# Optimization experiments

Hardware: AMD Instinct MI355X
Metric: run time of the kernel (lower is better)

Reference implementation:

```python
import jax, jax.numpy as jnp
import numpy as np


def _pair_indices(n_beads):
    # Replicates the torch loop ordering: all pairs at offset 1, then offset 2, ...
    i_list, j_list = [], []
    for off in range(1, n_beads):
        i = np.arange(n_beads - off)
        i_list.append(i)
        j_list.append(i + off)
    return np.concatenate(i_list), np.concatenate(j_list)


def setup_inputs() -> dict:
    key = jax.random.key(0)
    data = jax.random.normal(key, (4096, 128, 3), dtype=jnp.float32)
    return {"data": data}


def _features(data):
    n = data.shape[1]
    i_idx, j_idx = _pair_indices(n)  # static numpy index arrays

    # All pairwise distances, ordered by bead offset (matches torch loop order)
    dvec = data[:, j_idx, :] - data[:, i_idx, :]          # [B, P, 3]
    distances = jnp.linalg.norm(dvec, axis=2)             # [B, P]

    # Adjacent bond vectors: x[j+1] - x[j]
    adj = data[:, 1:, :] - data[:, :-1, :]                # [B, n-1, 3]

    # Planar angles over consecutive bond-vector pairs
    a0, a1 = adj[:, : n - 2, :], adj[:, 1 : n - 1, :]
    angles = jnp.arccos(
        jnp.sum(a0 * a1, axis=2)
        / jnp.linalg.norm(a0, axis=2)
        / jnp.linalg.norm(a1, axis=2)
    )                                                     # [B, n-2]

    # Dihedrals
    cpa = jnp.cross(a0, a1, axis=2)                       # [B, n-2, 3]
    plane = jnp.cross(cpa[:, 1 : n - 2, :], adj[:, 1 : n - 2, :], axis=2)  # [B, n-3, 3]
    c0, c1 = cpa[:, : n - 3, :], cpa[:, 1 : n - 2, :]
    nc0 = jnp.linalg.norm(c0, axis=2)
    dihedral_cos = jnp.sum(c0 * c1, axis=2) / nc0 / jnp.linalg.norm(c1, axis=2)
    p0 = plane[:, : n - 3, :]
    dihedral_sin = jnp.sum(c0 * p0, axis=2) / nc0 / jnp.linalg.norm(p0, axis=2)

    return jnp.concatenate([distances, angles, dihedral_cos, dihedral_sin], axis=1)


def reference(data):
    return _features(data)
```

## Files before the change

### kernel.cpp

```cpp
#include <hip/hip_runtime.h>
#include <math.h>

constexpr int NB    = 128;
constexpr int NPAIR = NB * (NB - 1) / 2;
constexpr int NANG  = NB - 2;
constexpr int NDIH  = NB - 3;
constexpr int ROW   = NPAIR + NANG + 2 * NDIH;

__global__ __launch_bounds__(128) void protein_feat_kernel(
        const float* __restrict__ data, float* __restrict__ out) {
    __shared__ float4 s4[NB];
    const int b = blockIdx.x;
    const int t = threadIdx.x;
    const float* src = data + (size_t)b * (NB * 3);

    s4[t] = make_float4(src[3 * t], src[3 * t + 1], src[3 * t + 2], 0.0f);
    __syncthreads();

    float* orow = out + (size_t)b * ROW;

    float px[4], py[4], pz[4];
    #pragma unroll
    for (int k = 0; k < 4; ++k) {
        int idx = t - k; if (idx < 0) idx = 0;
        float4 v = s4[idx];
        px[k] = v.x; py[k] = v.y; pz[k] = v.z;
    }

    int base = 0;
    for (int off = 1; off < NB; off += 4) {
        const int len = NB - off;
        int bk[4];
        bk[0] = base;
        bk[1] = bk[0] + len;
        bk[2] = bk[1] + len - 1;
        bk[3] = bk[2] + len - 2;
        base  = bk[3] + len - 3;
        if (t < len) {
            float4 pj = s4[t + off];
            #pragma unroll
            for (int k = 0; k < 4; ++k) {
                float dx = pj.x - px[k];
                float dy = pj.y - py[k];
                float dz = pj.z - pz[k];
                float d  = __builtin_amdgcn_sqrtf(dx * dx + dy * dy + dz * dz);
                if (t >= k)
                    orow[bk[k] + t - k] = d;
            }
        }
    }

    for (int v = t; v < NANG + 2 * NDIH; v += 128) {
        if (v < NANG) {
            int k = v;
            float4 p0 = s4[k], p1 = s4[k + 1], p2 = s4[k + 2];
            float a0x = p1.x - p0.x, a0y = p1.y - p0.y, a0z = p1.z - p0.z;
            float a1x = p2.x - p1.x, a1y = p2.y - p1.y, a1z = p2.z - p1.z;
            float d  = a0x * a1x + a0y * a1y + a0z * a1z;
            float r0 = rsqrtf(a0x * a0x + a0y * a0y + a0z * a0z);
            float r1 = rsqrtf(a1x * a1x + a1y * a1y + a1z * a1z);
            float c  = d * r0 * r1;
            c = fminf(1.0f, fmaxf(-1.0f, c));
            orow[NPAIR + k] = acosf(c);
        } else {
            int k = (v < NANG + NDIH) ? (v - NANG) : (v - NANG - NDIH);
            float4 p0 = s4[k], p1 = s4[k + 1], p2 = s4[k + 2], p3 = s4[k + 3];
            float e0x = p1.x - p0.x, e0y = p1.y - p0.y, e0z = p1.z - p0.z;
            float e1x = p2.x - p1.x, e1y = p2.y - p1.y, e1z = p2.z - p1.z;
            float e2x = p3.x - p2.x, e2y = p3.y - p2.y, e2z = p3.z - p2.z;
            float c0x = e0y * e1z - e0z * e1y;
            float c0y = e0z * e1x - e0x * e1z;
            float c0z = e0x * e1y - e0y * e1x;
            float c1x = e1y * e2z - e1z * e2y;
            float c1y = e1z * e2x - e1x * e2z;
            float c1z = e1x * e2y - e1y * e2x;
            float rn0 = rsqrtf(c0x * c0x + c0y * c0y + c0z * c0z);
            if (v < NANG + NDIH) {
                float d   = c0x * c1x + c0y * c1y + c0z * c1z;
                float rn1 = rsqrtf(c1x * c1x + c1y * c1y + c1z * c1z);
                orow[NPAIR + NANG + k] = d * rn0 * rn1;
            } else {
                float px_ = c1y * e1z - c1z * e1y;
                float py_ = c1z * e1x - c1x * e1z;
                float pz_ = c1x * e1y - c1y * e1x;
                float d  = c0x * px_ + c0y * py_ + c0z * pz_;
                float rp = rsqrtf(px_ * px_ + py_ * py_ + pz_ * pz_);
                orow[NPAIR + NANG + NDIH + k] = d * rn0 * rp;
            }
        }
    }
}

extern "C" void kernel_launch(void* const* d_in, const int* in_sizes, int n_in,
                              void* d_out, int out_size, void* d_ws, size_t ws_size,
                              hipStream_t stream) {
    const float* data = (const float*)d_in[0];
    float* out = (float*)d_out;
    const int batch = in_sizes[0] / (NB * 3);
    protein_feat_kernel<<<batch, 128, 0, stream>>>(data, out);
}
```

Baseline: 33.53 us.

## Split distance and angle work into separate kernels with occupancy hints

Splits the fused kernel into a pairwise-distance kernel and an angle/dihedral kernel, so the distance kernel no longer carries the register pressure of the transcendental angle code. Adds a min-blocks launch bound and unroll-by-2 on the distance loop, and unrolls the 4-way inner loop by hand. The cost is a second kernel launch that reloads the input and writes the angle and dihedral part of each row separately.

After: 37.20 us. 1.11x slower.

```diff
diff --git a/kernel.cpp b/kernel.cpp
--- a/kernel.cpp
+++ b/kernel.cpp
@@ -7,7 +7,7 @@
 constexpr int NDIH  = NB - 3;
 constexpr int ROW   = NPAIR + NANG + 2 * NDIH;
 
-__global__ __launch_bounds__(128) void protein_feat_kernel(
+__global__ __launch_bounds__(128, 8) void dist_kernel(
         const float* __restrict__ data, float* __restrict__ out) {
     __shared__ float4 s4[NB];
     const int b = blockIdx.x;
@@ -28,27 +28,44 @@
     }
 
     int base = 0;
+    #pragma unroll 2
     for (int off = 1; off < NB; off += 4) {
         const int len = NB - off;
-        int bk[4];
-        bk[0] = base;
-        bk[1] = bk[0] + len;
-        bk[2] = bk[1] + len - 1;
-        bk[3] = bk[2] + len - 2;
-        base  = bk[3] + len - 3;
+        int bk0 = base;
+        int bk1 = bk0 + len;
+        int bk2 = bk1 + len - 1;
+        int bk3 = bk2 + len - 2;
+        base    = bk3 + len - 3;
         if (t < len) {
             float4 pj = s4[t + off];
-            #pragma unroll
-            for (int k = 0; k < 4; ++k) {
-                float dx = pj.x - px[k];
-                float dy = pj.y - py[k];
-                float dz = pj.z - pz[k];
-                float d  = __builtin_amdgcn_sqrtf(dx * dx + dy * dy + dz * dz);
-                if (t >= k)
-                    orow[bk[k] + t - k] = d;
-            }
+            float dx, dy, dz, d;
+            dx = pj.x - px[0]; dy = pj.y - py[0]; dz = pj.z - pz[0];
+            d = __builtin_amdgcn_sqrtf(dx*dx + dy*dy + dz*dz);
+            orow[bk0 + t] = d;
+            dx = pj.x - px[1]; dy = pj.y - py[1]; dz = pj.z - pz[1];
+            d = __builtin_amdgcn_sqrtf(dx*dx + dy*dy + dz*dz);
+            if (t >= 1) orow[bk1 + t - 1] = d;
+            dx = pj.x - px[2]; dy = pj.y - py[2]; dz = pj.z - pz[2];
+            d = __builtin_amdgcn_sqrtf(dx*dx + dy*dy + dz*dz);
+            if (t >= 2) orow[bk2 + t - 2] = d;
+            dx = pj.x - px[3]; dy = pj.y - py[3]; dz = pj.z - pz[3];
+            d = __builtin_amdgcn_sqrtf(dx*dx + dy*dy + dz*dz);
+            if (t >= 3) orow[bk3 + t - 3] = d;
         }
     }
+}
+
+__global__ __launch_bounds__(128) void angle_kernel(
+        const float* __restrict__ data, float* __restrict__ out) {
+    __shared__ float4 s4[NB];
+    const int b = blockIdx.x;
+    const int t = threadIdx.x;
+    const float* src = data + (size_t)b * (NB * 3);
+
+    s4[t] = make_float4(src[3 * t], src[3 * t + 1], src[3 * t + 2], 0.0f);
+    __syncthreads();
+
+    float* orow = out + (size_t)b * ROW;
 
     for (int v = t; v < NANG + 2 * NDIH; v += 128) {
         if (v < NANG) {
@@ -80,11 +97,11 @@
                 float rn1 = rsqrtf(c1x * c1x + c1y * c1y + c1z * c1z);
                 orow[NPAIR + NANG + k] = d * rn0 * rn1;
             } else {
-                float px_ = c1y * e1z - c1z * e1y;
-                float py_ = c1z * e1x - c1x * e1z;
-                float pz_ = c1x * e1y - c1y * e1x;
-                float d  = c0x * px_ + c0y * py_ + c0z * pz_;
-                float rp = rsqrtf(px_ * px_ + py_ * py_ + pz_ * pz_);
+                float qx = c1y * e1z - c1z * e1y;
+                float qy = c1z * e1x - c1x * e1z;
+                float qz = c1x * e1y - c1y * e1x;
+                float d  = c0x * qx + c0y * qy + c0z * qz;
+                float rp = rsqrtf(qx * qx + qy * qy + qz * qz);
                 orow[NPAIR + NANG + NDIH + k] = d * rn0 * rp;
             }
         }
@@ -97,5 +114,6 @@
     const float* data = (const float*)d_in[0];
     float* out = (float*)d_out;
     const int batch = in_sizes[0] / (NB * 3);
-    protein_feat_kernel<<<batch, 128, 0, stream>>>(data, out);
+    dist_kernel<<<batch, 128, 0, stream>>>(data, out);
+    angle_kernel<<<batch, 128, 0, stream>>>(data, out);
 }
```
